# Optimization experiments

Hardware: AMD Instinct MI355X
Metric: run time of the kernel (lower is better)

## Reference

```python
import jax, jax.numpy as jnp
import numpy as np

B, C_IN, H, W = 4, 128, 32, 128   # W must equal out_channels (fc_out acts on last dim)
C_OUT, NUM_HEADS = 128, 2
BN_EPS = 1e-5


def setup_inputs() -> dict:
    key = jax.random.key(0)
    ks = jax.random.split(key, 14)
    s = 0.05  # small init scale for weights
    d = {
        "x": jax.random.normal(ks[0], (B, C_IN, H, W), jnp.float32),
        "wq": jax.random.normal(ks[1], (C_OUT, C_IN), jnp.float32) * s,
        "bq": jax.random.normal(ks[2], (C_OUT,), jnp.float32) * s,
        "wk": jax.random.normal(ks[3], (C_OUT, C_IN), jnp.float32) * s,
        "bk": jax.random.normal(ks[4], (C_OUT,), jnp.float32) * s,
        "wv": jax.random.normal(ks[5], (C_OUT, C_IN), jnp.float32) * s,
        "bv": jax.random.normal(ks[6], (C_OUT,), jnp.float32) * s,
        "fc_w": jax.random.normal(ks[7], (C_OUT, C_OUT), jnp.float32) * s,
        "fc_b": jax.random.normal(ks[8], (C_OUT,), jnp.float32) * s,
        "bn_gamma": jnp.ones((C_OUT,), jnp.float32),
        "bn_beta": jnp.zeros((C_OUT,), jnp.float32),
        "bn_mean": jax.random.normal(ks[9], (C_OUT,), jnp.float32) * 0.1,
        "bn_var": jax.random.uniform(ks[10], (C_OUT,), jnp.float32, 0.5, 1.5),
        "prelu_a": jnp.full((1,), 0.25, jnp.float32),
    }
    return d


def reference(x, wq, bq, wk, bk, wv, bv, fc_w, fc_b,
              bn_gamma, bn_beta, bn_mean, bn_var, prelu_a):
    b, c_in, h, w = x.shape
    c_out = wq.shape[0]
    nh = NUM_HEADS
    dk = c_out // nh
    L = h * w
    xf = x.reshape(b, c_in, L)                                # (B, Cin, L)
    # 1x1 convs == per-token linear projections
    q = jnp.einsum('oi,bil->bol', wq, xf) + bq[:, None]       # (B, Cout, L)
    k = jnp.einsum('oi,bil->bol', wk, xf) + bk[:, None]
    v = jnp.einsum('oi,bil->bol', wv, xf) + bv[:, None]
    Q = q.reshape(b, nh, dk, L)                               # (B, h, d_k, L)
    K = k.reshape(b, nh, dk, L)
    V = v.reshape(b, nh, dk, L)
    # scaled dot-product attention over the L = H*W tokens
    scores = jnp.einsum('bhdl,bhdm->bhlm', Q, K) / jnp.sqrt(jnp.float32(dk))
    attn = jax.nn.softmax(scores, axis=-1)                    # (B, h, L, L)
    out = jnp.einsum('bhlm,bhdm->bhdl', attn, V)              # (B, h, d_k, L)
    out = out.reshape(b, c_out, h, w)                         # (B, Cout, H, W)
    # fc_out: torch Linear on the LAST dim (W == Cout)
    y = jnp.einsum('bchw,ow->bcho', out, fc_w) + fc_b         # (B, Cout, H, W)
    # BatchNorm2d (eval mode: running stats) over channel dim
    inv = jax.lax.rsqrt(bn_var + BN_EPS)
    y = (y - bn_mean[None, :, None, None]) * (inv * bn_gamma)[None, :, None, None] \
        + bn_beta[None, :, None, None]
    # PReLU (single shared slope); dropout is identity in eval
    y = jnp.where(y > 0, y, prelu_a[0] * y)
    return y
```

## Files before the change

kernel.cpp:

```cpp
#include <hip/hip_runtime.h>

typedef _Float16 f16x8 __attribute__((ext_vector_type(8)));
typedef _Float16 f16x4t __attribute__((ext_vector_type(4)));
typedef __fp16 h16x2 __attribute__((ext_vector_type(2)));
typedef float f32x4 __attribute__((ext_vector_type(4)));
typedef float f32x16 __attribute__((ext_vector_type(16)));

#define L_SZ 4096

__device__ __forceinline__ unsigned short f2h(float f) {
    _Float16 h = (_Float16)f;
    return __builtin_bit_cast(unsigned short, h);
}
__device__ __forceinline__ unsigned int pk2(float a, float b) {
    h16x2 p = __builtin_amdgcn_cvt_pkrtz(a, b);
    return __builtin_bit_cast(unsigned int, p);
}

#define SLOT(row, ci) ((((ci) * 64) + ((row) & 32) + (((row) & 31) ^ (ci))) * 8)

__global__ __launch_bounds__(256) void cvt_kernel(
    const float* __restrict__ wq, const float* __restrict__ wk,
    const float* __restrict__ wv, const float* __restrict__ fcw_f,
    unsigned short* __restrict__ Wc, unsigned short* __restrict__ fcwh)
{
    int t = blockIdx.x * 256 + threadIdx.x;
    if (t < 16384)       Wc[t]          = f2h(wq[t]);
    else if (t < 32768)  Wc[t]          = f2h(wk[t - 16384]);
    else if (t < 49152)  Wc[t]          = f2h(wv[t - 32768]);
    else                 fcwh[t - 49152] = f2h(fcw_f[t - 49152]);
}

__global__ __launch_bounds__(256) void qkv_kernel(
    const float* __restrict__ x, const unsigned short* __restrict__ Wc,
    const float* __restrict__ bq, const float* __restrict__ bk, const float* __restrict__ bv,
    unsigned short* __restrict__ Qp, unsigned short* __restrict__ Kp,
    unsigned short* __restrict__ Vp)
{
    int blk = blockIdx.x;
    int proj = blk >> 9;
    int rem = blk & 511;
    int bidx = rem >> 7;
    int l0 = (rem & 127) * 32;
    int tid = threadIdx.x;
    int wave = tid >> 6, lane = tid & 63;
    int c = lane & 15, qd = lane >> 4;

    const float* bia = (proj == 0) ? bq : (proj == 1 ? bk : bv);

    __shared__ __align__(16) unsigned short Sh[5120];

    {
        int i  = tid >> 1;
        int lh = (tid & 1) * 16;
        const float* xs = &x[((size_t)bidx * 128 + i) * L_SZ + l0 + lh];
        float4 v0 = *(const float4*)xs;
        float4 v1 = *(const float4*)(xs + 4);
        float4 v2 = *(const float4*)(xs + 8);
        float4 v3 = *(const float4*)(xs + 12);
        float vv[16] = {v0.x,v0.y,v0.z,v0.w, v1.x,v1.y,v1.z,v1.w,
                        v2.x,v2.y,v2.z,v2.w, v3.x,v3.y,v3.z,v3.w};
        int ci = i >> 3, ij = i & 7;
        #pragma unroll
        for (int t = 0; t < 16; ++t) {
            int l = lh + t;
            Sh[l * 128 + ((ci ^ (l & 15)) * 8) + ij] = f2h(vv[t]);
        }
    }
    __syncthreads();

    f16x8 af[2][4];
    #pragma unroll
    for (int lt2 = 0; lt2 < 2; ++lt2)
        #pragma unroll
        for (int kc = 0; kc < 4; ++kc)
            af[lt2][kc] = *(const f16x8*)&Sh[(lt2 * 16 + c) * 128 + (((kc * 4 + qd) ^ c) * 8)];
    __syncthreads();

    f32x4 acc[2][2];
    #pragma unroll
    for (int lt2 = 0; lt2 < 2; ++lt2)
        #pragma unroll
        for (int nt = 0; nt < 2; ++nt) acc[lt2][nt] = (f32x4){0.f,0.f,0.f,0.f};

    const unsigned short* Wp = Wc + proj * 16384;
    #pragma unroll
    for (int kc = 0; kc < 4; ++kc) {
        #pragma unroll
        for (int nt = 0; nt < 2; ++nt) {
            int o = wave * 32 + nt * 16 + c;
            f16x8 bf = *(const f16x8*)&Wp[o * 128 + kc * 32 + qd * 8];
            acc[0][nt] = __builtin_amdgcn_mfma_f32_16x16x32_f16(af[0][kc], bf, acc[0][nt], 0, 0, 0);
            acc[1][nt] = __builtin_amdgcn_mfma_f32_16x16x32_f16(af[1][kc], bf, acc[1][nt], 0, 0, 0);
        }
    }

    const float s_q = 0.18033688011f;
    if (proj < 2) {
        #pragma unroll
        for (int lt2 = 0; lt2 < 2; ++lt2)
            #pragma unroll
            for (int nt = 0; nt < 2; ++nt) {
                int o = wave * 32 + nt * 16 + c;
                float bo = bia[o];
                #pragma unroll
                for (int r = 0; r < 4; ++r) {
                    float val = acc[lt2][nt][r] + bo;
                    if (proj == 0) val *= s_q;
                    Sh[(lt2 * 16 + qd * 4 + r) * 136 + o] = f2h(val);
                }
            }
        __syncthreads();
        unsigned short* dstp = (proj == 0) ? Qp : Kp;
        int l = tid >> 3, cp = tid & 7;
        int h = cp >> 2;
        uint4 q0 = *(const uint4*)&Sh[l * 136 + cp * 16];
        uint4 q1 = *(const uint4*)&Sh[l * 136 + cp * 16 + 8];
        unsigned short* d0 = &dstp[((size_t)(bidx * 2 + h) * L_SZ + l0 + l) * 64 + ((cp * 16) & 63)];
        *(uint4*)d0 = q0;
        *(uint4*)(d0 + 8) = q1;
    } else {
        #pragma unroll
        for (int lt2 = 0; lt2 < 2; ++lt2)
            #pragma unroll
            for (int nt = 0; nt < 2; ++nt) {
                int o = wave * 32 + nt * 16 + c;
                float bo = bia[o];
                #pragma unroll
                for (int r = 0; r < 4; ++r)
                    Sh[o * 40 + lt2 * 16 + qd * 4 + r] = f2h(acc[lt2][nt][r] + bo);
            }
        __syncthreads();
        int row = tid >> 1, half = (tid & 1) * 16;
        uint4 a0 = *(const uint4*)&Sh[row * 40 + half];
        uint4 a1 = *(const uint4*)&Sh[row * 40 + half + 8];
        unsigned short* d0 = &Vp[((size_t)(bidx * 128 + row)) * L_SZ + l0 + half];
        *(uint4*)d0 = a0;
        *(uint4*)(d0 + 8) = a1;
    }
}

__global__ __launch_bounds__(256, 3) void attn_kernel(
    const unsigned short* __restrict__ Qp, const unsigned short* __restrict__ Kp,
    const unsigned short* __restrict__ Vp,
    unsigned short* __restrict__ Opart, float* __restrict__ Mpart, float* __restrict__ Lpart)
{
    int blk = blockIdx.x;
    int lt = blk & 31;
    int bh = (blk >> 5) & 7;
    int sp = blk >> 8;
    int l0 = lt * 128;
    int tid = threadIdx.x;
    int wave = tid >> 6, lane = tid & 63;
    int ln = lane & 31, hi = lane >> 5;
    int b = bh >> 1, h = bh & 1;

    __shared__ __align__(16) unsigned short Ks[2][4096];
    __shared__ __align__(16) unsigned short Vs[2][4096];
    __shared__ __align__(16) unsigned short Ps[4][2048];

    const unsigned short* Qb = Qp + (size_t)bh * L_SZ * 64;
    const unsigned short* Kb = Kp + (size_t)bh * L_SZ * 64;
    const unsigned short* Vb = Vp + ((size_t)b * 128 + h * 64) * L_SZ;

    int lq = l0 + wave * 32 + ln;
    f16x8 qf[4];
    #pragma unroll
    for (int kc = 0; kc < 4; ++kc)
        qf[kc] = *(const f16x8*)&Qb[(size_t)lq * 64 + kc * 16 + hi * 8];

    float m_st = -1e30f, lsum = 0.f;
    f32x16 acc0 = {}, acc1 = {};

    int urow = tid >> 3, uci = tid & 7;
    int mglob = sp * 1024;

    uint4 kreg[2], vreg[2];
    #pragma unroll
    for (int j = 0; j < 2; ++j) {
        int row = urow + j * 32;
        kreg[j] = *(const uint4*)&Kb[(size_t)(mglob + row) * 64 + uci * 8];
        vreg[j] = *(const uint4*)&Vb[(size_t)row * L_SZ + mglob + uci * 8];
    }
    #pragma unroll
    for (int j = 0; j < 2; ++j) {
        int row = urow + j * 32;
        *(uint4*)&Ks[0][SLOT(row, uci)] = kreg[j];
        *(uint4*)&Vs[0][SLOT(row, uci)] = vreg[j];
    }

    for (int it = 0; it < 16; ++it) {
        int cur = it & 1;
        __syncthreads();
        if (it < 15) {
            int m0 = mglob + (it + 1) * 64;
            #pragma unroll
            for (int j = 0; j < 2; ++j) {
                int row = urow + j * 32;
                kreg[j] = *(const uint4*)&Kb[(size_t)(m0 + row) * 64 + uci * 8];
                vreg[j] = *(const uint4*)&Vb[(size_t)row * L_SZ + m0 + uci * 8];
            }
        }

        f32x16 s0 = {}, s1 = {};
        #pragma unroll
        for (int kc = 0; kc < 4; ++kc) {
            int cd = kc * 2 + hi;
            f16x8 k0 = *(const f16x8*)&Ks[cur][SLOT(ln, cd)];
            f16x8 k1 = *(const f16x8*)&Ks[cur][SLOT(32 + ln, cd)];
            s0 = __builtin_amdgcn_mfma_f32_32x32x16_f16(k0, qf[kc], s0, 0, 0, 0);
            s1 = __builtin_amdgcn_mfma_f32_32x32x16_f16(k1, qf[kc], s1, 0, 0, 0);
        }

        float mx = s0[0];
        #pragma unroll
        for (int r = 1; r < 16; ++r) mx = fmaxf(mx, s0[r]);
        #pragma unroll
        for (int r = 0; r < 16; ++r) mx = fmaxf(mx, s1[r]);
        mx = fmaxf(mx, __shfl_xor(mx, 32));
        if (__any(mx > m_st)) {
            float mnew = fmaxf(m_st, mx);
            float alpha = exp2f(m_st - mnew);
            m_st = mnew;
            lsum *= alpha;
            #pragma unroll
            for (int r = 0; r < 16; ++r) { acc0[r] *= alpha; acc1[r] *= alpha; }
        }
        float rsum = 0.f;
        #pragma unroll
        for (int r = 0; r < 16; ++r) { float p = exp2f(s0[r] - m_st); s0[r] = p; rsum += p; }
        #pragma unroll
        for (int r = 0; r < 16; ++r) { float p = exp2f(s1[r] - m_st); s1[r] = p; rsum += p; }
        lsum += rsum;

        #pragma unroll
        for (int g = 0; g < 4; ++g) {
            uint2 w0;
            w0.x = pk2(s0[g * 4 + 0], s0[g * 4 + 1]);
            w0.y = pk2(s0[g * 4 + 2], s0[g * 4 + 3]);
            *(uint2*)&Ps[wave][(g * 32 + (ln ^ g)) * 8 + hi * 4] = w0;
            int g2 = 4 + g;
            uint2 w1;
            w1.x = pk2(s1[g * 4 + 0], s1[g * 4 + 1]);
            w1.y = pk2(s1[g * 4 + 2], s1[g * 4 + 3]);
            *(uint2*)&Ps[wave][(g2 * 32 + (ln ^ g2)) * 8 + hi * 4] = w1;
        }

        #pragma unroll
        for (int kc = 0; kc < 4; ++kc) {
            int cd = kc * 2 + hi;
            f16x8 pf = *(const f16x8*)&Ps[wave][(cd * 32 + (ln ^ cd)) * 8];
            f16x8 v0 = *(const f16x8*)&Vs[cur][SLOT(ln, cd)];
            f16x8 v1 = *(const f16x8*)&Vs[cur][SLOT(32 + ln, cd)];
            acc0 = __builtin_amdgcn_mfma_f32_32x32x16_f16(v0, pf, acc0, 0, 0, 0);
            acc1 = __builtin_amdgcn_mfma_f32_32x32x16_f16(v1, pf, acc1, 0, 0, 0);
        }

        if (it < 15) {
            #pragma unroll
            for (int j = 0; j < 2; ++j) {
                int row = urow + j * 32;
                *(uint4*)&Ks[cur ^ 1][SLOT(row, uci)] = kreg[j];
                *(uint4*)&Vs[cur ^ 1][SLOT(row, uci)] = vreg[j];
            }
        }
    }

    float l_tot = lsum + __shfl_xor(lsum, 32);
    unsigned short* Ow = Opart + (size_t)(sp * 8 + bh) * 64 * 4096;
    #pragma unroll
    for (int r = 0; r < 16; ++r) {
        int d0 = (r & 3) + 8 * (r >> 2) + 4 * hi;
        Ow[(size_t)d0 * 4096 + lq] = f2h(acc0[r]);
        Ow[(size_t)(32 + d0) * 4096 + lq] = f2h(acc1[r]);
    }
    if (hi == 0) {
        Mpart[(sp * 8 + bh) * 4096 + lq] = m_st;
        Lpart[(sp * 8 + bh) * 4096 + lq] = l_tot;
    }
}

__global__ __launch_bounds__(256) void scale_kernel(
    const float* __restrict__ Mp, const float* __restrict__ Lp,
    unsigned short* __restrict__ Scl)
{
    int t = blockIdx.x * 256 + threadIdx.x;
    float m[4], l[4];
    #pragma unroll
    for (int s = 0; s < 4; ++s) { m[s] = Mp[s * 32768 + t]; l[s] = Lp[s * 32768 + t]; }
    float mx = fmaxf(fmaxf(m[0], m[1]), fmaxf(m[2], m[3]));
    float a[4], den = 0.f;
    #pragma unroll
    for (int s = 0; s < 4; ++s) { a[s] = exp2f(m[s] - mx); den += a[s] * l[s]; }
    float inv = 1.0f / den;
    uint2 sc;
    sc.x = pk2(a[0] * inv, a[1] * inv);
    sc.y = pk2(a[2] * inv, a[3] * inv);
    *(uint2*)&Scl[t * 4] = sc;
}

__global__ __launch_bounds__(256) void fc_kernel(
    const unsigned short* __restrict__ Opart, const unsigned short* __restrict__ Scl,
    const unsigned short* __restrict__ fcwh, const float* __restrict__ fc_b,
    const float* __restrict__ bn_g, const float* __restrict__ bn_b,
    const float* __restrict__ bn_m, const float* __restrict__ bn_v,
    const float* __restrict__ prelu_a, float* __restrict__ out)
{
    int blk = blockIdx.x;
    int b = blk >> 7, ch = blk & 127;
    int bh = b * 2 + (ch >> 6);
    int d = ch & 63;
    int tid = threadIdx.x;
    int wave = tid >> 6, lane = tid & 63;
    int c = lane & 15, qd = lane >> 4;
    int hhb = (wave >> 1) * 16;
    int nb = (wave & 1) * 64;
    int h_tok = hhb + c;

    size_t obase = (size_t)bh * 262144 + (size_t)d * 4096 + h_tok * 128;
    int sbase = (bh << 12) + h_tok * 128;

    f16x8 af[4];
    #pragma unroll
    for (int kc = 0; kc < 4; ++kc) {
        int w0 = kc * 32 + qd * 8;
        f16x8 ov[4];
        #pragma unroll
        for (int s = 0; s < 4; ++s)
            ov[s] = *(const f16x8*)&Opart[(size_t)s * 2097152 + obase + w0];
        #pragma unroll
        for (int j = 0; j < 8; ++j) {
            f16x4t sc = *(const f16x4t*)&Scl[(sbase + w0 + j) * 4];
            float v = (float)ov[0][j] * (float)sc[0] + (float)ov[1][j] * (float)sc[1]
                    + (float)ov[2][j] * (float)sc[2] + (float)ov[3][j] * (float)sc[3];
            af[kc][j] = (_Float16)v;
        }
    }

    f32x4 acc[4];
    #pragma unroll
    for (int nt = 0; nt < 4; ++nt) acc[nt] = (f32x4){0.f,0.f,0.f,0.f};
    #pragma unroll
    for (int kc = 0; kc < 4; ++kc) {
        #pragma unroll
        for (int nt = 0; nt < 4; ++nt) {
            int o = nb + nt * 16 + c;
            f16x8 bf = *(const f16x8*)&fcwh[o * 128 + kc * 32 + qd * 8];
            acc[nt] = __builtin_amdgcn_mfma_f32_16x16x32_f16(af[kc], bf, acc[nt], 0, 0, 0);
        }
    }

    float pa = prelu_a[0];
    float g  = bn_g[ch] * rsqrtf(bn_v[ch] + 1e-5f);
    float mn = bn_m[ch], bt = bn_b[ch];
    size_t rbase = ((size_t)(b * 128 + ch)) * 32;
    #pragma unroll
    for (int r = 0; r < 4; ++r) {
        size_t orow = rbase + hhb + qd * 4 + r;
        #pragma unroll
        for (int nt = 0; nt < 4; ++nt) {
            int o = nb + nt * 16 + c;
            float y = (acc[nt][r] + fc_b[o] - mn) * g + bt;
            y = y > 0.f ? y : pa * y;
            out[orow * 128 + o] = y;
        }
    }
}

extern "C" void kernel_launch(void* const* d_in, const int* in_sizes, int n_in,
                              void* d_out, int out_size, void* d_ws, size_t ws_size,
                              hipStream_t stream) {
    const float* x     = (const float*)d_in[0];
    const float* wq    = (const float*)d_in[1];
    const float* bq    = (const float*)d_in[2];
    const float* wk    = (const float*)d_in[3];
    const float* bk    = (const float*)d_in[4];
    const float* wv    = (const float*)d_in[5];
    const float* bv    = (const float*)d_in[6];
    const float* fcw_f = (const float*)d_in[7];
    const float* fcb   = (const float*)d_in[8];
    const float* bn_g  = (const float*)d_in[9];
    const float* bn_b  = (const float*)d_in[10];
    const float* bn_m  = (const float*)d_in[11];
    const float* bn_v  = (const float*)d_in[12];
    const float* pa    = (const float*)d_in[13];
    float* out = (float*)d_out;

    unsigned short* Wc    = (unsigned short*)d_ws;
    unsigned short* fcwh  = Wc + 49152;
    unsigned short* Qp    = fcwh + 16384;
    unsigned short* Kp    = Qp + 2097152;
    unsigned short* Vp    = Kp + 2097152;
    unsigned short* Opart = Vp + 2097152;
    float* Mpart = (float*)(Opart + 8388608);
    float* Lpart = Mpart + 131072;
    unsigned short* Scl = (unsigned short*)(Lpart + 131072);

    hipLaunchKernelGGL(cvt_kernel,   dim3(256),  dim3(256), 0, stream,
                       wq, wk, wv, fcw_f, Wc, fcwh);
    hipLaunchKernelGGL(qkv_kernel,   dim3(1536), dim3(256), 0, stream,
                       x, Wc, bq, bk, bv, Qp, Kp, Vp);
    hipLaunchKernelGGL(attn_kernel,  dim3(1024), dim3(256), 0, stream,
                       Qp, Kp, Vp, Opart, Mpart, Lpart);
    hipLaunchKernelGGL(scale_kernel, dim3(128),  dim3(256), 0, stream,
                       Mpart, Lpart, Scl);
    hipLaunchKernelGGL(fc_kernel,    dim3(512),  dim3(256), 0, stream,
                       Opart, Scl, fcwh, fcb, bn_g, bn_b, bn_m, bn_v, pa, out);
}
```

Baseline: 178.5 us.

## Build P fragments in registers via cross-lane shuffles instead of LDS round trip

The softmax probabilities no longer go through a per-wave shared-memory buffer. They are packed to fp16 and rearranged into the MFMA B-operand layout with xor-32 lane shuffles. The row max and row sum reductions become tree reductions, which shortens the serial dependency chains. This removes LDS writes and reads plus the shared-memory footprint, which may allow higher occupancy, at the cost of extra shuffle and select instructions.

Measured after the change: 177.1 us. Within noise of the previous version (-0.8%).

```diff
diff --git a/kernel.cpp b/kernel.cpp
--- a/kernel.cpp
+++ b/kernel.cpp
@@ -157,7 +157,6 @@
 
     __shared__ __align__(16) unsigned short Ks[2][4096];
     __shared__ __align__(16) unsigned short Vs[2][4096];
-    __shared__ __align__(16) unsigned short Ps[4][2048];
 
     const unsigned short* Qb = Qp + (size_t)bh * L_SZ * 64;
     const unsigned short* Kb = Kp + (size_t)bh * L_SZ * 64;
@@ -212,11 +211,14 @@
             s1 = __builtin_amdgcn_mfma_f32_32x32x16_f16(k1, qf[kc], s1, 0, 0, 0);
         }
 
-        float mx = s0[0];
-        #pragma unroll
-        for (int r = 1; r < 16; ++r) mx = fmaxf(mx, s0[r]);
-        #pragma unroll
-        for (int r = 0; r < 16; ++r) mx = fmaxf(mx, s1[r]);
+        float t[16];
+        #pragma unroll
+        for (int r = 0; r < 16; ++r) t[r] = fmaxf(s0[r], s1[r]);
+        #pragma unroll
+        for (int r = 0; r < 8; ++r) t[r] = fmaxf(t[r], t[r + 8]);
+        #pragma unroll
+        for (int r = 0; r < 4; ++r) t[r] = fmaxf(t[r], t[r + 4]);
+        float mx = fmaxf(fmaxf(t[0], t[1]), fmaxf(t[2], t[3]));
         mx = fmaxf(mx, __shfl_xor(mx, 32));
         if (__any(mx > m_st)) {
             float mnew = fmaxf(m_st, mx);
@@ -226,30 +228,42 @@
             #pragma unroll
             for (int r = 0; r < 16; ++r) { acc0[r] *= alpha; acc1[r] *= alpha; }
         }
-        float rsum = 0.f;
-        #pragma unroll
-        for (int r = 0; r < 16; ++r) { float p = exp2f(s0[r] - m_st); s0[r] = p; rsum += p; }
-        #pragma unroll
-        for (int r = 0; r < 16; ++r) { float p = exp2f(s1[r] - m_st); s1[r] = p; rsum += p; }
-        lsum += rsum;
-
+        #pragma unroll
+        for (int r = 0; r < 16; ++r) { s0[r] = exp2f(s0[r] - m_st); s1[r] = exp2f(s1[r] - m_st); }
+        float u[16];
+        #pragma unroll
+        for (int r = 0; r < 16; ++r) u[r] = s0[r] + s1[r];
+        #pragma unroll
+        for (int r = 0; r < 8; ++r) u[r] += u[r + 8];
+        #pragma unroll
+        for (int r = 0; r < 4; ++r) u[r] += u[r + 4];
+        lsum += (u[0] + u[1]) + (u[2] + u[3]);
+
+        uint4 pfrag[4];
         #pragma unroll
         for (int g = 0; g < 4; ++g) {
-            uint2 w0;
-            w0.x = pk2(s0[g * 4 + 0], s0[g * 4 + 1]);
-            w0.y = pk2(s0[g * 4 + 2], s0[g * 4 + 3]);
-            *(uint2*)&Ps[wave][(g * 32 + (ln ^ g)) * 8 + hi * 4] = w0;
-            int g2 = 4 + g;
-            uint2 w1;
-            w1.x = pk2(s1[g * 4 + 0], s1[g * 4 + 1]);
-            w1.y = pk2(s1[g * 4 + 2], s1[g * 4 + 3]);
-            *(uint2*)&Ps[wave][(g2 * 32 + (ln ^ g2)) * 8 + hi * 4] = w1;
-        }
-
-        #pragma unroll
-        for (int kc = 0; kc < 4; ++kc) {
-            int cd = kc * 2 + hi;
-            f16x8 pf = *(const f16x8*)&Ps[wave][(cd * 32 + (ln ^ cd)) * 8];
+            const float* sv = (g < 2) ? (const float*)&s0 : (const float*)&s1;
+            int br = (g & 1) * 8;
+            unsigned int pax = pk2(sv[br + 0], sv[br + 1]);
+            unsigned int pay = pk2(sv[br + 2], sv[br + 3]);
+            unsigned int pbx = pk2(sv[br + 4], sv[br + 5]);
+            unsigned int pby = pk2(sv[br + 6], sv[br + 7]);
+            unsigned int sx = hi ? pax : pbx;
+            unsigned int sy = hi ? pay : pby;
+            unsigned int rx = __shfl_xor(sx, 32);
+            unsigned int ry = __shfl_xor(sy, 32);
+            uint4 f;
+            f.x = hi ? rx : pax;
+            f.y = hi ? ry : pay;
+            f.z = hi ? pbx : rx;
+            f.w = hi ? pby : ry;
+            pfrag[g] = f;
+        }
+
+        #pragma unroll
+        for (int mb = 0; mb < 4; ++mb) {
+            int cd = mb * 2 + hi;
+            f16x8 pf = __builtin_bit_cast(f16x8, pfrag[mb]);
             f16x8 v0 = *(const f16x8*)&Vs[cur][SLOT(ln, cd)];
             f16x8 v1 = *(const f16x8*)&Vs[cur][SLOT(32 + ln, cd)];
             acc0 = __builtin_amdgcn_mfma_f32_32x32x16_f16(v0, pf, acc0, 0, 0, 0);
```
